# Optimization experiments

Hardware: AMD Instinct MI355X
Metric: run time of the kernel (lower is better)

## Reference

```python
import jax, jax.numpy as jnp
import numpy as np

jax.config.update("jax_enable_x64", True)

# Dimensions (see shape_source): grouped per-filter valid conv, stride 1
F, H, W, CIN = 64, 256, 256, 64
KH = KW = 3
HO, WO = H - KH + 1, W - KW + 1
L = 1  # acc is independent of the last output dim l in the original loop


def setup_inputs() -> dict:
    key = jax.random.key(0)
    k1, k2, k3 = jax.random.split(key, 3)
    # int8-valued tensors, stored as int8 like the original (dtype str 'int8')
    x = jax.random.randint(k1, (F, H, W, CIN), -128, 128, dtype=jnp.int32).astype(jnp.int8)
    w = jax.random.randint(k2, (F, KH, KW, CIN), -128, 128, dtype=jnp.int32).astype(jnp.int8)
    bias = jax.random.randint(k3, (F,), -1024, 1024, dtype=jnp.int32)
    return {
        "x": x,
        "w": w,
        "bias": bias,
        "q_mantissa": 1340958551,  # typical TFLite requant mantissa (Q31)
        "exponent": -11,
        "output_zero_point": -3,
    }


def reference(x, w, bias, q_mantissa, exponent, output_zero_point):
    # int8 -> int32 accumulation (faithful to np.int32 acc in original)
    x32 = x.astype(jnp.int32)
    w32 = w.astype(jnp.int32)
    # acc[i,j,k] = sum_{m,n,o} x[i, j+m, k+n, o] * w[i, m, n, o]
    acc = jnp.zeros((F, HO, WO), dtype=jnp.int32)
    for m in range(KH):
        for n in range(KW):
            acc = acc + jnp.einsum(
                'fjko,fo->fjk', x32[:, m:m + HO, n:n + WO, :], w32[:, m, n, :]
            )
    acc = acc + bias[:, None, None]

    # multiply_by_quantize_mul: fixed-point requantization with rounding shift
    if q_mantissa < 2147418112:
        reduced_mantissa = (q_mantissa + (1 << 15)) >> 16  # python precedence: (q + 2^15) >> 16
    else:
        reduced_mantissa = 32767
    total_shifts = 15 - exponent
    acc64 = acc.astype(jnp.int64) * np.int64(reduced_mantissa)
    acc64 = acc64 + (np.int64(1) << (total_shifts - 1))  # rounding bit
    res = jnp.right_shift(acc64, total_shifts)

    res = res + output_zero_point
    res = jnp.clip(res, -128, 127).astype(jnp.int8)
    # original writes the same acc for every l in output_shape[3]
    return jnp.broadcast_to(res[..., None], (F, HO, WO, L))
```

## Files before the change

kernel.cpp:

```cpp
#include <hip/hip_runtime.h>
#include <cstdint>
#include <cstddef>

#define NF 64
#define NH 256
#define NW 256
#define NC 64
#define HOUT 254
#define WOUT 254
#define JR 32
#define NCHUNK 8
#define NBLK (NF * NCHUNK)

__global__ void detect_kernel(const unsigned int* __restrict__ x,
                              int* __restrict__ flagp) {
    if (threadIdx.x != 0 || blockIdx.x != 0) return;
    int c32 = 0, cf = 0;
    for (int i = 0; i < 64; ++i) {
        unsigned int v = x[i];
        unsigned int hi = v >> 8;
        if (hi == 0u || hi == 0x00FFFFFFu) c32++;
        float f = __uint_as_float(v);
        if (f == truncf(f) && f >= -129.0f && f <= 128.0f &&
            (v == 0u || fabsf(f) >= 1.0f)) cf++;
    }
    flagp[0] = (c32 == 64) ? 1 : ((cf == 64) ? 2 : 0);
}

__device__ __forceinline__ int dot4(int a, int b, int c) {
#if __has_builtin(__builtin_amdgcn_sdot4)
    return __builtin_amdgcn_sdot4(a, b, c, false);
#else
    #pragma unroll
    for (int i = 0; i < 4; ++i)
        c += (int)(signed char)(a >> (8 * i)) * (int)(signed char)(b >> (8 * i));
    return c;
#endif
}

__device__ __forceinline__ int pack4(const int* p) {
    int4 v = *(const int4*)p;
    return (v.x & 255) | ((v.y & 255) << 8) | ((v.z & 255) << 16) | (v.w << 24);
}
__device__ __forceinline__ int pack4(const float* p) {
    float4 v = *(const float4*)p;
    int a = (int)v.x, b = (int)v.y, c = (int)v.z, d = (int)v.w;
    return (a & 255) | ((b & 255) << 8) | ((c & 255) << 16) | (d << 24);
}

template <typename T>
__device__ __forceinline__ void conv_body(
    const T* __restrict__ x, const T* __restrict__ w,
    const int* __restrict__ bias, const int* __restrict__ qmp,
    const int* __restrict__ exp_p, const int* __restrict__ zpp,
    int* __restrict__ out) {
    __shared__ int xlds[4 * 4096];
    __shared__ int wlds[144];

    const int tid = threadIdx.x;
    const int bid = blockIdx.x;
    const int f = bid >> 3;
    const int j0 = (bid & 7) * JR;
    const int nout = min(JR, HOUT - j0);

    if (tid < 144) wlds[tid] = pack4(w + (size_t)f * 576 + tid * 4);
    __syncthreads();

    int4 W[9][4];
    #pragma unroll
    for (int t = 0; t < 9; ++t)
        #pragma unroll
        for (int q4 = 0; q4 < 4; ++q4)
            W[t][q4] = *(const int4*)&wlds[t * 16 + q4 * 4];

    const int qm = qmp[0], ex = exp_p[0], zp = zpp[0];
    const int rmant = (qm < 2147418112) ? ((qm + 32768) >> 16) : 32767;
    const int tsh = 15 - ex;
    const long long rnd = 1LL << (tsh - 1);
    const int bv = bias[f];
    const int k = tid;

    for (int r = 0; r < nout + 2; ++r) {
        {
            const T* xr = x + (size_t)(f * NH + (j0 + r)) * (NW * NC);
            int* dst = xlds + (r & 3) * 4096;
            #pragma unroll
            for (int i = 0; i < 16; ++i) {
                int g = i * 256 + tid;
                int packed = pack4(xr + (size_t)g * 4);
                int col = g >> 4, q = g & 15;
                dst[(q >> 2) * 1024 + col * 4 + (q & 3)] = packed;
            }
        }
        __syncthreads();
        if (r >= 2 && k < WOUT) {
            const int jo = j0 + r - 2;
            int a0 = 0, a1 = 0, a2 = 0, a3 = 0;
            #pragma unroll
            for (int m = 0; m < 3; ++m) {
                const int4* bm = (const int4*)(xlds + ((r - 2 + m) & 3) * 4096);
                #pragma unroll
                for (int n = 0; n < 3; ++n) {
                    #pragma unroll
                    for (int q4 = 0; q4 < 4; ++q4) {
                        int4 xv = bm[q4 * 256 + k + n];
                        int4 wv = W[m * 3 + n][q4];
                        a0 = dot4(xv.x, wv.x, a0);
                        a1 = dot4(xv.y, wv.y, a1);
                        a2 = dot4(xv.z, wv.z, a2);
                        a3 = dot4(xv.w, wv.w, a3);
                    }
                }
            }
            long long a = (long long)(a0 + a1 + a2 + a3 + bv) * rmant + rnd;
            long long res = (a >> tsh) + zp;
            res = res < -128 ? -128 : (res > 127 ? 127 : res);
            out[((size_t)f * HOUT + jo) * WOUT + k] = (int)res;
        }
    }
}

__global__ __launch_bounds__(256, 2) void conv_i32(
    const int* __restrict__ x, const int* __restrict__ w,
    const int* __restrict__ bias, const int* __restrict__ qmp,
    const int* __restrict__ exp_p, const int* __restrict__ zpp,
    int* __restrict__ out, const int* __restrict__ flagp) {
    if (flagp[0] != 1) return;
    conv_body<int>(x, w, bias, qmp, exp_p, zpp, out);
}

__global__ __launch_bounds__(256, 2) void conv_f32(
    const float* __restrict__ x, const float* __restrict__ w,
    const int* __restrict__ bias, const int* __restrict__ qmp,
    const int* __restrict__ exp_p, const int* __restrict__ zpp,
    int* __restrict__ out, const int* __restrict__ flagp) {
    if (flagp[0] != 2) return;
    conv_body<float>(x, w, bias, qmp, exp_p, zpp, out);
}

extern "C" void kernel_launch(void* const* d_in, const int* in_sizes, int n_in,
                              void* d_out, int out_size, void* d_ws,
                              size_t ws_size, hipStream_t stream) {
    (void)in_sizes; (void)n_in; (void)ws_size; (void)out_size;
    const void* x = d_in[0];
    const void* w = d_in[1];
    const int* bias = (const int*)d_in[2];
    const int* qm = (const int*)d_in[3];
    const int* ex = (const int*)d_in[4];
    const int* zp = (const int*)d_in[5];
    int* out = (int*)d_out;
    int* flagp = (int*)d_ws;

    detect_kernel<<<1, 64, 0, stream>>>((const unsigned int*)x, flagp);
    conv_i32<<<NBLK, 256, 0, stream>>>((const int*)x, (const int*)w,
                                       bias, qm, ex, zp, out, flagp);
    conv_f32<<<NBLK, 256, 0, stream>>>((const float*)x, (const float*)w,
                                       bias, qm, ex, zp, out, flagp);
}
```

Baseline: 1.359 ms.

## Prefetch next input row into registers while computing current row

Software-pipelines the row loads: the next row of x is issued into registers before the dot-product compute and packed and stored to LDS on the following iteration, so global load latency overlaps with compute. The load pattern changes so each thread reads 64 contiguous channels of one column (four 16-byte loads) and writes one int4 to LDS, instead of 16 scattered packs. Weights are now read from LDS in the inner loop rather than held in 144 registers, which frees registers for the prefetch buffer at the cost of extra LDS traffic.

```diff
diff --git a/kernel.cpp b/kernel.cpp
--- a/kernel.cpp
+++ b/kernel.cpp
@@ -9,8 +9,7 @@
 #define HOUT 254
 #define WOUT 254
 #define JR 32
-#define NCHUNK 8
-#define NBLK (NF * NCHUNK)
+#define NBLK (NF * 8)
 
 __global__ void detect_kernel(const unsigned int* __restrict__ x,
                               int* __restrict__ flagp) {
@@ -38,14 +37,17 @@
 #endif
 }
 
-__device__ __forceinline__ int pack4(const int* p) {
-    int4 v = *(const int4*)p;
-    return (v.x & 255) | ((v.y & 255) << 8) | ((v.z & 255) << 16) | (v.w << 24);
+template <typename T> struct V4;
+template <> struct V4<int>   { using t = int4; };
+template <> struct V4<float> { using t = float4; };
+
+__device__ __forceinline__ int pk(int4 v) {
+    return (v.x & 255) | ((v.y & 255) << 8) | ((v.z & 255) << 16) |
+           ((v.w & 255) << 24);
 }
-__device__ __forceinline__ int pack4(const float* p) {
-    float4 v = *(const float4*)p;
-    int a = (int)v.x, b = (int)v.y, c = (int)v.z, d = (int)v.w;
-    return (a & 255) | ((b & 255) << 8) | ((c & 255) << 16) | (d << 24);
+__device__ __forceinline__ int pk(float4 v) {
+    return ((int)v.x & 255) | (((int)v.y & 255) << 8) |
+           (((int)v.z & 255) << 16) | (((int)v.w & 255) << 24);
 }
 
 template <typename T>
@@ -62,39 +64,62 @@
     const int f = bid >> 3;
     const int j0 = (bid & 7) * JR;
     const int nout = min(JR, HOUT - j0);
+    using VT = typename V4<T>::t;
 
-    if (tid < 144) wlds[tid] = pack4(w + (size_t)f * 576 + tid * 4);
-    __syncthreads();
-
-    int4 W[9][4];
-    #pragma unroll
-    for (int t = 0; t < 9; ++t)
-        #pragma unroll
-        for (int q4 = 0; q4 < 4; ++q4)
-            W[t][q4] = *(const int4*)&wlds[t * 16 + q4 * 4];
+    if (tid < 144) {
+        VT v = *(const VT*)(w + (size_t)f * 576 + tid * 4);
+        wlds[tid] = pk(v);
+    }
 
     const int qm = qmp[0], ex = exp_p[0], zp = zpp[0];
     const int rmant = (qm < 2147418112) ? ((qm + 32768) >> 16) : 32767;
     const int tsh = 15 - ex;
     const long long rnd = 1LL << (tsh - 1);
     const int bv = bias[f];
-    const int k = tid;
+    const size_t rowstride = (size_t)NW * NC;
+    const T* xs = x + ((size_t)f * NH + j0) * rowstride;
 
-    for (int r = 0; r < nout + 2; ++r) {
+    int4 P[4];
+    {
+        VT L[16];
+        #pragma unroll
+        for (int i = 0; i < 4; ++i) {
+            const int c = i * 256 + tid;
+            #pragma unroll
+            for (int jj = 0; jj < 4; ++jj)
+                L[i * 4 + jj] = *(const VT*)(xs + (size_t)c * 16 + jj * 4);
+        }
+        #pragma unroll
+        for (int i = 0; i < 4; ++i)
+            P[i] = make_int4(pk(L[i * 4]), pk(L[i * 4 + 1]),
+                             pk(L[i * 4 + 2]), pk(L[i * 4 + 3]));
+    }
+
+    for (int r = 0; r <= nout + 1; ++r) {
         {
-            const T* xr = x + (size_t)(f * NH + (j0 + r)) * (NW * NC);
             int* dst = xlds + (r & 3) * 4096;
             #pragma unroll
-            for (int i = 0; i < 16; ++i) {
-                int g = i * 256 + tid;
-                int packed = pack4(xr + (size_t)g * 4);
-                int col = g >> 4, q = g & 15;
-                dst[(q >> 2) * 1024 + col * 4 + (q & 3)] = packed;
+            for (int i = 0; i < 4; ++i) {
+                const int c = i * 256 + tid;
+                *(int4*)&dst[(c & 3) * 1024 + (c >> 2) * 4] = P[i];
             }
         }
         __syncthreads();
-        if (r >= 2 && k < WOUT) {
-            const int jo = j0 + r - 2;
+
+        const bool more = (r + 1 <= nout + 1);
+        VT L[16];
+        if (more) {
+            const T* src = xs + (size_t)(r + 1) * rowstride;
+            #pragma unroll
+            for (int i = 0; i < 4; ++i) {
+                const int c = i * 256 + tid;
+                #pragma unroll
+                for (int jj = 0; jj < 4; ++jj)
+                    L[i * 4 + jj] = *(const VT*)(src + (size_t)c * 16 + jj * 4);
+            }
+        }
+
+        if (r >= 2 && tid < WOUT) {
             int a0 = 0, a1 = 0, a2 = 0, a3 = 0;
             #pragma unroll
             for (int m = 0; m < 3; ++m) {
@@ -103,8 +128,8 @@
                 for (int n = 0; n < 3; ++n) {
                     #pragma unroll
                     for (int q4 = 0; q4 < 4; ++q4) {
-                        int4 xv = bm[q4 * 256 + k + n];
-                        int4 wv = W[m * 3 + n][q4];
+                        int4 xv = bm[q4 * 256 + tid + n];
+                        int4 wv = *(const int4*)&wlds[(m * 3 + n) * 16 + q4 * 4];
                         a0 = dot4(xv.x, wv.x, a0);
                         a1 = dot4(xv.y, wv.y, a1);
                         a2 = dot4(xv.z, wv.z, a2);
@@ -115,7 +140,14 @@
             long long a = (long long)(a0 + a1 + a2 + a3 + bv) * rmant + rnd;
             long long res = (a >> tsh) + zp;
             res = res < -128 ? -128 : (res > 127 ? 127 : res);
-            out[((size_t)f * HOUT + jo) * WOUT + k] = (int)res;
+            out[((size_t)f * HOUT + (j0 + r - 2)) * WOUT + tid] = (int)res;
+        }
+
+        if (more) {
+            #pragma unroll
+            for (int i = 0; i < 4; ++i)
+                P[i] = make_int4(pk(L[i * 4]), pk(L[i * 4 + 1]),
+                                 pk(L[i * 4 + 2]), pk(L[i * 4 + 3]));
         }
     }
 }
```

New measurement: 1.368 ms. No clear change (+0.7%).
